# Optimization experiments

Measured on AMD Instinct MI355X. Metric: run time of the kernel, lower is better.

## Reference

```python
import jax, jax.numpy as jnp
import numpy as np

TAU = 1.0

def setup_inputs() -> dict:
    key = jax.random.key(0)
    scores = jax.random.normal(key, (16, 2048), dtype=jnp.float32)
    return {"scores": scores}

def reference(scores) -> jnp.ndarray:
    # scores: [B, n]
    B, n = scores.shape
    s = scores[:, :, None]                                  # [B, n, 1]
    # pairwise abs differences |s_i - s_j|
    A = jnp.abs(s - jnp.swapaxes(s, 1, 2))                  # [B, n, n]
    # torch: matmul(matmul(A, ones), ones^T) == row-sums broadcast over cols
    Bsum = jnp.sum(A, axis=-1, keepdims=True)               # [B, n, 1]
    # scaling_j = n + 1 - 2*(j+1)
    scaling = (n + 1 - 2 * (jnp.arange(n) + 1)).astype(scores.dtype)  # [n]
    C = s * scaling[None, None, :]                          # [B, n, n]
    P_max = jnp.swapaxes(C - Bsum, 1, 2)                    # [B, n, n]
    P_hat = jax.nn.softmax(P_max / TAU, axis=-1)
    return P_hat
```

## Files before the change

### kernel.cpp

```cpp
#include <hip/hip_runtime.h>
#include <math.h>

#define N 2048
#define BATCH 16

__global__ __launch_bounds__(128) void bsum_kernel(const float* __restrict__ scores,
                                                   float* __restrict__ dsum) {
    __shared__ float s_sh[N];
    const int b = blockIdx.x >> 4;
    const int jBase = (blockIdx.x & 15) * 128;
    const float* s = scores + (size_t)b * N;

    for (int t = threadIdx.x; t < N / 4; t += 128) {
        ((float4*)s_sh)[t] = ((const float4*)s)[t];
    }
    __syncthreads();

    const int j = jBase + threadIdx.x;
    const float sj = s_sh[j];
    float acc = 0.f;
#pragma unroll 8
    for (int k = 0; k < N / 4; ++k) {
        float4 v = ((const float4*)s_sh)[k];
        acc += fabsf(sj - v.x) + fabsf(sj - v.y) + fabsf(sj - v.z) + fabsf(sj - v.w);
    }
    dsum[(size_t)b * N + j] = acc;
}

__global__ __launch_bounds__(256) void softmax_kernel(const float* __restrict__ scores,
                                                      const float* __restrict__ dsum,
                                                      float* __restrict__ out) {
    __shared__ float s_sh[N];
    __shared__ float d_sh[N];

    const int blocksPerBatch = N / 4;
    const int b = blockIdx.x / blocksPerBatch;
    const int blockRow = blockIdx.x % blocksPerBatch;

    const float* s = scores + (size_t)b * N;
    const float* dd = dsum + (size_t)b * N;

    for (int t = threadIdx.x; t < N / 4; t += 256) {
        ((float4*)s_sh)[t] = ((const float4*)s)[t];
        ((float4*)d_sh)[t] = ((const float4*)dd)[t];
    }
    __syncthreads();

    const int wave = threadIdx.x >> 6;
    const int lane = threadIdx.x & 63;
    const int row = blockRow * 4 + wave;
    const float c = (float)(N - 1 - 2 * row);

    float lg[32];
    float m = -INFINITY;
#pragma unroll
    for (int it = 0; it < 8; ++it) {
        const int idx = it * 64 + lane;
        float4 s4 = ((const float4*)s_sh)[idx];
        float4 d4 = ((const float4*)d_sh)[idx];
        float l0 = fmaf(c, s4.x, -d4.x);
        float l1 = fmaf(c, s4.y, -d4.y);
        float l2 = fmaf(c, s4.z, -d4.z);
        float l3 = fmaf(c, s4.w, -d4.w);
        lg[it * 4 + 0] = l0;
        lg[it * 4 + 1] = l1;
        lg[it * 4 + 2] = l2;
        lg[it * 4 + 3] = l3;
        m = fmaxf(m, fmaxf(fmaxf(l0, l1), fmaxf(l2, l3)));
    }
#pragma unroll
    for (int off = 32; off > 0; off >>= 1)
        m = fmaxf(m, __shfl_xor(m, off, 64));

    float sum = 0.f;
#pragma unroll
    for (int k = 0; k < 32; ++k) {
        lg[k] = __expf(lg[k] - m);
        sum += lg[k];
    }
#pragma unroll
    for (int off = 32; off > 0; off >>= 1)
        sum += __shfl_xor(sum, off, 64);

    const float inv = 1.0f / sum;

    float* orow = out + (((size_t)b * N) + row) * N;
#pragma unroll
    for (int it = 0; it < 8; ++it) {
        const int idx = it * 64 + lane;
        float4 o;
        o.x = lg[it * 4 + 0] * inv;
        o.y = lg[it * 4 + 1] * inv;
        o.z = lg[it * 4 + 2] * inv;
        o.w = lg[it * 4 + 3] * inv;
        ((float4*)orow)[idx] = o;
    }
}

extern "C" void kernel_launch(void* const* d_in, const int* in_sizes, int n_in,
                              void* d_out, int out_size, void* d_ws, size_t ws_size,
                              hipStream_t stream) {
    const float* scores = (const float*)d_in[0];
    float* out = (float*)d_out;
    float* dsum = (float*)d_ws;

    bsum_kernel<<<BATCH * 16, 128, 0, stream>>>(scores, dsum);
    softmax_kernel<<<BATCH * (N / 4), 256, 0, stream>>>(scores, dsum, out);
}
```

Before: 269.3 us.

## Split bsum reduction across waves, reuse row inputs per wave, nontemporal output stores

```diff
diff --git a/kernel.cpp b/kernel.cpp
--- a/kernel.cpp
+++ b/kernel.cpp
@@ -4,96 +4,104 @@
 #define N 2048
 #define BATCH 16
 
-__global__ __launch_bounds__(128) void bsum_kernel(const float* __restrict__ scores,
-                                                   float* __restrict__ dsum) {
+typedef float vfloat4 __attribute__((ext_vector_type(4)));
+
+__global__ __launch_bounds__(512) void bsum_kernel(const float* __restrict__ scores,
+                                                   float* __restrict__ ndsum) {
     __shared__ float s_sh[N];
+    __shared__ float part[4][128];
     const int b = blockIdx.x >> 4;
     const int jBase = (blockIdx.x & 15) * 128;
     const float* s = scores + (size_t)b * N;
 
-    for (int t = threadIdx.x; t < N / 4; t += 128) {
-        ((float4*)s_sh)[t] = ((const float4*)s)[t];
-    }
+    ((float4*)s_sh)[threadIdx.x] = ((const float4*)s)[threadIdx.x];
     __syncthreads();
 
-    const int j = jBase + threadIdx.x;
-    const float sj = s_sh[j];
+    const int jl = threadIdx.x & 127;
+    const int q  = threadIdx.x >> 7;
+    const float sj = s_sh[jBase + jl];
+    const int k4Base = q * (N / 16);
+
     float acc = 0.f;
 #pragma unroll 8
-    for (int k = 0; k < N / 4; ++k) {
-        float4 v = ((const float4*)s_sh)[k];
+    for (int k4 = 0; k4 < N / 16; ++k4) {
+        float4 v = ((const float4*)s_sh)[k4Base + k4];
         acc += fabsf(sj - v.x) + fabsf(sj - v.y) + fabsf(sj - v.z) + fabsf(sj - v.w);
     }
-    dsum[(size_t)b * N + j] = acc;
+    part[q][jl] = acc;
+    __syncthreads();
+
+    if (threadIdx.x < 128) {
+        float d = part[0][threadIdx.x] + part[1][threadIdx.x] +
+                  part[2][threadIdx.x] + part[3][threadIdx.x];
+        ndsum[(size_t)b * N + jBase + threadIdx.x] = -d;
+    }
 }
 
-__global__ __launch_bounds__(256) void softmax_kernel(const float* __restrict__ scores,
-                                                      const float* __restrict__ dsum,
-                                                      float* __restrict__ out) {
-    __shared__ float s_sh[N];
-    __shared__ float d_sh[N];
-
-    const int blocksPerBatch = N / 4;
-    const int b = blockIdx.x / blocksPerBatch;
-    const int blockRow = blockIdx.x % blocksPerBatch;
-
-    const float* s = scores + (size_t)b * N;
-    const float* dd = dsum + (size_t)b * N;
-
-    for (int t = threadIdx.x; t < N / 4; t += 256) {
-        ((float4*)s_sh)[t] = ((const float4*)s)[t];
-        ((float4*)d_sh)[t] = ((const float4*)dd)[t];
-    }
-    __syncthreads();
-
+__global__ __launch_bounds__(256, 4) void softmax_kernel(const float* __restrict__ scores,
+                                                         const float* __restrict__ ndsum,
+                                                         float* __restrict__ out) {
+    const int b = blockIdx.x >> 6;
     const int wave = threadIdx.x >> 6;
     const int lane = threadIdx.x & 63;
-    const int row = blockRow * 4 + wave;
-    const float c = (float)(N - 1 - 2 * row);
+    const int rowBase = (blockIdx.x & 63) * 32 + wave * 8;
 
-    float lg[32];
-    float m = -INFINITY;
+    const float* s  = scores + (size_t)b * N;
+    const float* nd = ndsum  + (size_t)b * N;
+
+    float4 s4[8], nd4[8];
 #pragma unroll
     for (int it = 0; it < 8; ++it) {
         const int idx = it * 64 + lane;
-        float4 s4 = ((const float4*)s_sh)[idx];
-        float4 d4 = ((const float4*)d_sh)[idx];
-        float l0 = fmaf(c, s4.x, -d4.x);
-        float l1 = fmaf(c, s4.y, -d4.y);
-        float l2 = fmaf(c, s4.z, -d4.z);
-        float l3 = fmaf(c, s4.w, -d4.w);
-        lg[it * 4 + 0] = l0;
-        lg[it * 4 + 1] = l1;
-        lg[it * 4 + 2] = l2;
-        lg[it * 4 + 3] = l3;
-        m = fmaxf(m, fmaxf(fmaxf(l0, l1), fmaxf(l2, l3)));
+        s4[it]  = ((const float4*)s)[idx];
+        nd4[it] = ((const float4*)nd)[idx];
     }
+
+    float* obase = out + ((size_t)b * N + rowBase) * N;
+
+#pragma unroll 1
+    for (int r = 0; r < 8; ++r) {
+        const float c = (float)(N - 1 - 2 * (rowBase + r));
+        float lg[32];
+        float m = -INFINITY;
 #pragma unroll
-    for (int off = 32; off > 0; off >>= 1)
-        m = fmaxf(m, __shfl_xor(m, off, 64));
+        for (int it = 0; it < 8; ++it) {
+            float l0 = fmaf(c, s4[it].x, nd4[it].x);
+            float l1 = fmaf(c, s4[it].y, nd4[it].y);
+            float l2 = fmaf(c, s4[it].z, nd4[it].z);
+            float l3 = fmaf(c, s4[it].w, nd4[it].w);
+            lg[it * 4 + 0] = l0;
+            lg[it * 4 + 1] = l1;
+            lg[it * 4 + 2] = l2;
+            lg[it * 4 + 3] = l3;
+            m = fmaxf(m, fmaxf(fmaxf(l0, l1), fmaxf(l2, l3)));
+        }
+#pragma unroll
+        for (int off = 32; off > 0; off >>= 1)
+            m = fmaxf(m, __shfl_xor(m, off, 64));
 
-    float sum = 0.f;
+        float sum = 0.f;
 #pragma unroll
-    for (int k = 0; k < 32; ++k) {
-        lg[k] = __expf(lg[k] - m);
-        sum += lg[k];
-    }
+        for (int k = 0; k < 32; ++k) {
+            lg[k] = __expf(lg[k] - m);
+            sum += lg[k];
+        }
 #pragma unroll
-    for (int off = 32; off > 0; off >>= 1)
-        sum += __shfl_xor(sum, off, 64);
+        for (int off = 32; off > 0; off >>= 1)
+            sum += __shfl_xor(sum, off, 64);
 
-    const float inv = 1.0f / sum;
+        const float inv = __builtin_amdgcn_rcpf(sum);
 
-    float* orow = out + (((size_t)b * N) + row) * N;
+        float* orow = obase + (size_t)r * N;
 #pragma unroll
-    for (int it = 0; it < 8; ++it) {
-        const int idx = it * 64 + lane;
-        float4 o;
-        o.x = lg[it * 4 + 0] * inv;
-        o.y = lg[it * 4 + 1] * inv;
-        o.z = lg[it * 4 + 2] * inv;
-        o.w = lg[it * 4 + 3] * inv;
-        ((float4*)orow)[idx] = o;
+        for (int it = 0; it < 8; ++it) {
+            vfloat4 o;
+            o.x = lg[it * 4 + 0] * inv;
+            o.y = lg[it * 4 + 1] * inv;
+            o.z = lg[it * 4 + 2] * inv;
+            o.w = lg[it * 4 + 3] * inv;
+            __builtin_nontemporal_store(o, (vfloat4*)orow + (it * 64 + lane));
+        }
     }
 }
 
@@ -102,8 +110,8 @@
                               hipStream_t stream) {
     const float* scores = (const float*)d_in[0];
     float* out = (float*)d_out;
-    float* dsum = (float*)d_ws;
+    float* ndsum = (float*)d_ws;
 
-    bsum_kernel<<<BATCH * 16, 128, 0, stream>>>(scores, dsum);
-    softmax_kernel<<<BATCH * (N / 4), 256, 0, stream>>>(scores, dsum, out);
+    bsum_kernel<<<BATCH * 16, 512, 0, stream>>>(scores, ndsum);
+    softmax_kernel<<<BATCH * 64, 256, 0, stream>>>(scores, ndsum, out);
 }
```

Measured after the change: 268.9 us. About the same (-0.2%).
